# Performance work log

Hardware: AMD Instinct MI355X
Metric: run time of the kernel (lower is better)

## Reference

```python
import jax, jax.numpy as jnp
import numpy as np

FEATURE_DIM = 128
VALUE_DIM = 128


def setup_inputs() -> dict:
    key = jax.random.key(0)
    k1, k2, k3 = jax.random.split(key, 3)
    BH, S = 32, 4096
    q = jax.random.normal(k1, (BH, S, FEATURE_DIM), dtype=jnp.float32)
    k = jax.random.normal(k2, (BH, S, FEATURE_DIM), dtype=jnp.float32)
    v = jax.random.normal(k3, (BH, S, VALUE_DIM), dtype=jnp.float32)
    return {"q": q, "k": k, "v": v, "chunk_size": 128}


def reference(q, k, v, chunk_size):
    # q,k: [BH,S,F]; v: [BH,S,V]. Chunked fast-weight linear-attention scan:
    # out_t = q_t . (sum_{s<=t} k_s (x) v_s) / t
    BH, S, F = q.shape
    V = v.shape[-1]
    C = max(1, int(chunk_size))
    assert S % C == 0, "seq_len must be divisible by chunk_size for this reference"
    n_chunks = S // C
    # [n_chunks, BH, C, dim] for lax.scan over chunks
    qc = q.reshape(BH, n_chunks, C, F).transpose(1, 0, 2, 3)
    kc = k.reshape(BH, n_chunks, C, F).transpose(1, 0, 2, 3)
    vc = v.reshape(BH, n_chunks, C, V).transpose(1, 0, 2, 3)

    w0 = jnp.zeros((BH, F, V), dtype=q.dtype)

    def step(w_state, inputs):
        qi, ki, vi = inputs  # [BH,C,F], [BH,C,F], [BH,C,V]
        kv = jnp.einsum('bnf,bnv->bnfv', ki, vi)          # [BH,C,F,V]
        w_prefix = jnp.cumsum(kv, axis=1) + w_state[:, None]  # inclusive prefix sums
        out = jnp.einsum('bnf,bnfv->bnv', qi, w_prefix)    # [BH,C,V]
        return w_prefix[:, -1], out

    _, outs = jax.lax.scan(step, w0, (qc, kc, vc))
    out = outs.transpose(1, 0, 2, 3).reshape(BH, S, V)
    inv_counts = 1.0 / jnp.arange(1, S + 1, dtype=q.dtype)
    return out * inv_counts[None, :, None]
```

## Files before the change

### kernel.cpp

```cpp
#include <hip/hip_runtime.h>


typedef _Float16 f16;
typedef __attribute__((ext_vector_type(4))) _Float16 f16x4;
typedef __attribute__((ext_vector_type(8))) _Float16 f16x8;
typedef __attribute__((ext_vector_type(4))) float f32x4;
typedef __attribute__((ext_vector_type(16))) float f32x16;
typedef __attribute__((ext_vector_type(4))) float fv4;

#define MFMA32(a, b, c) __builtin_amdgcn_mfma_f32_32x32x16_f16((a), (b), (c), 0, 0, 0)

__device__ __forceinline__ int swzb(int row, int col) {
  int s = (row ^ (row >> 3)) & 7;
  return (row << 8) + ((col << 1) ^ (s << 4));
}

__device__ __forceinline__ f16x8 frag32(const f16* lds, int row, int kk, int lane) {
  int c0 = (kk << 4) + ((lane >> 5) << 3);
  return *(const f16x8*)((const char*)lds + swzb(row, c0));
}

__device__ __forceinline__ int rowf(int r, int g) {
  return (r & 3) + ((r >> 2) << 3) + (g << 2);
}

__global__ __launch_bounds__(512, 1)
void ttr_pt(const float* __restrict__ k, const float* __restrict__ v,
            f16* __restrict__ pt) {
  __shared__ f16 kT[128 * 128];
  __shared__ f16 vT[128 * 128];
  const int tid = threadIdx.x, lane = tid & 63, wave = tid >> 6;
  const int bh = blockIdx.x >> 5, c = blockIdx.x & 31;
  const float* kg = k + ((size_t)bh * 4096 + c * 128) * 128;
  const float* vg = v + ((size_t)bh * 4096 + c * 128) * 128;
  const int f0 = (tid & 31) << 2;
#pragma unroll
  for (int p = 0; p < 8; ++p) {
    int s = (p << 4) + (tid >> 5);
    fv4 xk = *(const fv4*)(kg + s * 128 + f0);
    fv4 xv = *(const fv4*)(vg + s * 128 + f0);
#pragma unroll
    for (int e = 0; e < 4; ++e) {
      *(f16*)((char*)kT + swzb(f0 + e, s)) = (f16)xk[e];
      *(f16*)((char*)vT + swzb(f0 + e, s)) = (f16)xv[e];
    }
  }
  __syncthreads();
  const int l31 = lane & 31, g = lane >> 5;
  const int mt = wave >> 1, nt0 = (wave & 1) << 1;
  f32x16 p0 = {0.f}, p1 = {0.f};
#pragma unroll
  for (int kk = 0; kk < 8; ++kk) {
    f16x8 a = frag32(vT, (mt << 5) + l31, kk, lane);
    p0 = MFMA32(a, frag32(kT, (nt0 << 5) + l31, kk, lane), p0);
    p1 = MFMA32(a, frag32(kT, ((nt0 + 1) << 5) + l31, kk, lane), p1);
  }
  f16* dst = pt + (size_t)blockIdx.x * 16384;
#pragma unroll
  for (int r = 0; r < 16; ++r) {
    int vr = (mt << 5) + rowf(r, g);
    dst[vr * 128 + (nt0 << 5) + l31] = (f16)p0[r];
    dst[vr * 128 + ((nt0 + 1) << 5) + l31] = (f16)p1[r];
  }
}

__global__ __launch_bounds__(256, 1)
void ttr_prefix(const f16* __restrict__ pt, f16* __restrict__ w) {
  __shared__ f16 xch[256 * 8];
  const int tid = threadIdx.x;
  const int bh = blockIdx.x >> 3, vs = blockIdx.x & 7;
  const int v0 = vs << 4;
  const int NT = v0 >> 5;
  const int vloc = tid >> 4, fblk = tid & 15;
  const size_t bhbase = (size_t)bh * 32 * 16384;
  const f16* src = pt + bhbase + (size_t)(v0 + vloc) * 128 + fblk * 8;
  const int kk = tid >> 5, gg = (tid >> 4) & 1, lc = tid & 15;
  f16* dstu = w + bhbase +
              (size_t)(((NT * 8 + kk) * 64) + gg * 32 + (v0 & 31) + lc) * 8;
  const int phi_w = vloc * 16 + (fblk ^ vloc);
  const int phi_r = lc * 16 + ((tid >> 4) ^ lc);
  float acc[8];
#pragma unroll
  for (int e = 0; e < 8; ++e) acc[e] = 0.f;
  for (int c = 0; c < 32; ++c) {
    f16x8 pcur = *(const f16x8*)(src + (size_t)c * 16384);
    f16x8 h;
#pragma unroll
    for (int e = 0; e < 8; ++e) h[e] = (f16)acc[e];
    *(f16x8*)(xch + phi_w * 8) = h;
    __syncthreads();
    f16x8 o = *(const f16x8*)(xch + phi_r * 8);
    *(f16x8*)(dstu + (size_t)c * 16384) = o;
    __syncthreads();
#pragma unroll
    for (int e = 0; e < 8; ++e) acc[e] += (float)pcur[e];
  }
}

__global__ __launch_bounds__(256, 3)
void ttr_out(const float* __restrict__ q, const float* __restrict__ k,
             const float* __restrict__ v, const f16* __restrict__ w,
             float* __restrict__ out) {
  __shared__ f16 s_lds[128 * 128];
  __shared__ f16 vT[32 * 128];
  __shared__ f16 w_lds[512 * 8];
  const int tid = threadIdx.x, lane = tid & 63, wave = tid >> 6;
  const int l31 = lane & 31, g = lane >> 5;
  const int widx = blockIdx.x & 31;
  const int gidx = ((blockIdx.x >> 5) << 3) + (widx & 7);
  const int vq = widx >> 3;
  const int bh = gidx >> 5, c = gidx & 31;
  const float* qg = q + ((size_t)bh * 4096 + c * 128) * 128;
  const float* kg = k + ((size_t)bh * 4096 + c * 128) * 128;
  const float* vg = v + ((size_t)bh * 4096 + c * 128) * 128 + vq * 32;

  const f16* wsrc = w + (size_t)gidx * 16384 + vq * 4096;
  f16x8 wl0 = *(const f16x8*)(wsrc + tid * 8);
  f16x8 wl1 = *(const f16x8*)(wsrc + (256 + tid) * 8);

  f16x8 qf[8];
  {
    const float* qr = qg + ((wave << 5) + l31) * 128 + (g << 3);
#pragma unroll
    for (int kk = 0; kk < 8; ++kk) {
      fv4 a = *(const fv4*)(qr + (kk << 4));
      fv4 b = *(const fv4*)(qr + (kk << 4) + 4);
      f16x8 h = {(f16)a[0], (f16)a[1], (f16)a[2], (f16)a[3],
                 (f16)b[0], (f16)b[1], (f16)b[2], (f16)b[3]};
      qf[kk] = h;
    }
  }
  {
    const int c0 = (tid & 31) << 2;
#pragma unroll
    for (int p = 0; p < 16; ++p) {
      int s = (p << 3) + (tid >> 5);
      fv4 xk = *(const fv4*)(kg + s * 128 + c0);
      f16x4 hk = {(f16)xk[0], (f16)xk[1], (f16)xk[2], (f16)xk[3]};
      *(f16x4*)((char*)s_lds + swzb(s, c0)) = hk;
    }
  }
  {
    const int c0 = (tid & 7) << 2;
#pragma unroll
    for (int p = 0; p < 4; ++p) {
      int s = (p << 5) + (tid >> 3);
      fv4 xv = *(const fv4*)(vg + s * 128 + c0);
#pragma unroll
      for (int e = 0; e < 4; ++e)
        *(f16*)((char*)vT + swzb(c0 + e, s)) = (f16)xv[e];
    }
  }
  *(f16x8*)(w_lds + tid * 8) = wl0;
  *(f16x8*)(w_lds + (256 + tid) * 8) = wl1;
  __syncthreads();

  f32x16 s0 = {0.f}, s1 = {0.f}, s2 = {0.f}, s3 = {0.f}, o0 = {0.f};
#pragma unroll
  for (int kk = 0; kk < 8; ++kk) {
    f16x8 aq = qf[kk];
    s0 = MFMA32(aq, frag32(s_lds, l31, kk, lane), s0);
    if (wave >= 1) s1 = MFMA32(aq, frag32(s_lds, 32 + l31, kk, lane), s1);
    if (wave >= 2) s2 = MFMA32(aq, frag32(s_lds, 64 + l31, kk, lane), s2);
    if (wave >= 3) s3 = MFMA32(aq, frag32(s_lds, 96 + l31, kk, lane), s3);
  }
  __syncthreads();

#define STORE_S(ACC, J)                                                       \
  {                                                                           \
    const bool dg = ((J) == wave);                                            \
    _Pragma("unroll") for (int r = 0; r < 16; ++r) {                          \
      int rl = rowf(r, g);                                                    \
      float val = ACC[r];                                                     \
      if (dg && l31 > rl) val = 0.f;                                          \
      *(f16*)((char*)s_lds + swzb((wave << 5) + rl, ((J) << 5) + l31)) =      \
          (f16)val;                                                           \
    }                                                                         \
  }
  STORE_S(s0, 0);
  if (wave >= 1) STORE_S(s1, 1);
  if (wave >= 2) STORE_S(s2, 2);
  if (wave >= 3) STORE_S(s3, 3);

#pragma unroll
  for (int kk = 0; kk < 8; ++kk)
    o0 = MFMA32(qf[kk], *(const f16x8*)(w_lds + ((kk << 6) + lane) * 8), o0);

  const int nkk = (wave + 1) << 1;
  for (int kk = 0; kk < nkk; ++kk)
    o0 = MFMA32(frag32(s_lds, (wave << 5) + l31, kk, lane),
                frag32(vT, l31, kk, lane), o0);

  float* og = out + (((size_t)bh * 4096) + c * 128 + (wave << 5)) * 128 + vq * 32;
#pragma unroll
  for (int r = 0; r < 16; ++r) {
    int rl = rowf(r, g);
    float tg = (float)(c * 128 + (wave << 5) + rl + 1);
    og[rl * 128 + l31] = o0[r] * __builtin_amdgcn_rcpf(tg);
  }
}

extern "C" void kernel_launch(void* const* d_in, const int* in_sizes, int n_in,
                              void* d_out, int out_size, void* d_ws, size_t ws_size,
                              hipStream_t stream) {
  const float* q = (const float*)d_in[0];
  const float* k = (const float*)d_in[1];
  const float* v = (const float*)d_in[2];
  float* o = (float*)d_out;
  f16* pt = (f16*)d_ws;
  f16* w = pt + (size_t)32 * 32 * 16384;
  ttr_pt<<<dim3(1024), dim3(512), 0, stream>>>(k, v, pt);
  ttr_prefix<<<dim3(256), dim3(256), 0, stream>>>(pt, w);
  ttr_out<<<dim3(4096), dim3(256), 0, stream>>>(q, k, v, w, o);
}
```

Before: 107.1 us.

## Load W fragments directly into registers, drop W LDS staging, raise occupancy

The output kernel now loads the prefix-state W fragments straight from global memory into registers, in the MFMA layout, instead of staging them through shared memory. The inter-chunk q·W product is issued before the first barrier so it overlaps with the LDS fill. Conversions to fp16 now use packed round-toward-zero cvt_pkrtz, and launch bounds ask for 4 blocks per CU instead of 3. The costs are more register pressure under the tighter bound, which could spill, and a change in rounding mode from round-to-nearest to round-toward-zero.

Measured after the change: 212.0 us. 98.0% more time.

```diff
diff --git a/kernel.cpp b/kernel.cpp
--- a/kernel.cpp
+++ b/kernel.cpp
@@ -2,13 +2,19 @@
 
 
 typedef _Float16 f16;
+typedef __attribute__((ext_vector_type(2))) _Float16 f16x2;
 typedef __attribute__((ext_vector_type(4))) _Float16 f16x4;
 typedef __attribute__((ext_vector_type(8))) _Float16 f16x8;
-typedef __attribute__((ext_vector_type(4))) float f32x4;
 typedef __attribute__((ext_vector_type(16))) float f32x16;
 typedef __attribute__((ext_vector_type(4))) float fv4;
 
 #define MFMA32(a, b, c) __builtin_amdgcn_mfma_f32_32x32x16_f16((a), (b), (c), 0, 0, 0)
+
+__device__ __forceinline__ f16x4 cvt4(fv4 x) {
+  f16x2 lo = __builtin_bit_cast(f16x2, __builtin_amdgcn_cvt_pkrtz(x[0], x[1]));
+  f16x2 hi = __builtin_bit_cast(f16x2, __builtin_amdgcn_cvt_pkrtz(x[2], x[3]));
+  return __builtin_shufflevector(lo, hi, 0, 1, 2, 3);
+}
 
 __device__ __forceinline__ int swzb(int row, int col) {
   int s = (row ^ (row >> 3)) & 7;
@@ -97,13 +103,12 @@
   }
 }
 
-__global__ __launch_bounds__(256, 3)
+__global__ __launch_bounds__(256, 4)
 void ttr_out(const float* __restrict__ q, const float* __restrict__ k,
              const float* __restrict__ v, const f16* __restrict__ w,
              float* __restrict__ out) {
   __shared__ f16 s_lds[128 * 128];
   __shared__ f16 vT[32 * 128];
-  __shared__ f16 w_lds[512 * 8];
   const int tid = threadIdx.x, lane = tid & 63, wave = tid >> 6;
   const int l31 = lane & 31, g = lane >> 5;
   const int widx = blockIdx.x & 31;
@@ -115,19 +120,19 @@
   const float* vg = v + ((size_t)bh * 4096 + c * 128) * 128 + vq * 32;
 
   const f16* wsrc = w + (size_t)gidx * 16384 + vq * 4096;
-  f16x8 wl0 = *(const f16x8*)(wsrc + tid * 8);
-  f16x8 wl1 = *(const f16x8*)(wsrc + (256 + tid) * 8);
+  f16x8 wf[8];
+#pragma unroll
+  for (int kk = 0; kk < 8; ++kk)
+    wf[kk] = *(const f16x8*)(wsrc + (size_t)((kk << 6) + lane) * 8);
 
   f16x8 qf[8];
   {
     const float* qr = qg + ((wave << 5) + l31) * 128 + (g << 3);
 #pragma unroll
     for (int kk = 0; kk < 8; ++kk) {
-      fv4 a = *(const fv4*)(qr + (kk << 4));
-      fv4 b = *(const fv4*)(qr + (kk << 4) + 4);
-      f16x8 h = {(f16)a[0], (f16)a[1], (f16)a[2], (f16)a[3],
-                 (f16)b[0], (f16)b[1], (f16)b[2], (f16)b[3]};
-      qf[kk] = h;
+      f16x4 a = cvt4(*(const fv4*)(qr + (kk << 4)));
+      f16x4 b = cvt4(*(const fv4*)(qr + (kk << 4) + 4));
+      qf[kk] = __builtin_shufflevector(a, b, 0, 1, 2, 3, 4, 5, 6, 7);
     }
   }
   {
@@ -135,9 +140,7 @@
 #pragma unroll
     for (int p = 0; p < 16; ++p) {
       int s = (p << 3) + (tid >> 5);
-      fv4 xk = *(const fv4*)(kg + s * 128 + c0);
-      f16x4 hk = {(f16)xk[0], (f16)xk[1], (f16)xk[2], (f16)xk[3]};
-      *(f16x4*)((char*)s_lds + swzb(s, c0)) = hk;
+      *(f16x4*)((char*)s_lds + swzb(s, c0)) = cvt4(*(const fv4*)(kg + s * 128 + c0));
     }
   }
   {
@@ -151,11 +154,12 @@
         *(f16*)((char*)vT + swzb(c0 + e, s)) = (f16)xv[e];
     }
   }
-  *(f16x8*)(w_lds + tid * 8) = wl0;
-  *(f16x8*)(w_lds + (256 + tid) * 8) = wl1;
+  f32x16 o0 = {0.f};
+#pragma unroll
+  for (int kk = 0; kk < 8; ++kk) o0 = MFMA32(qf[kk], wf[kk], o0);
   __syncthreads();
 
-  f32x16 s0 = {0.f}, s1 = {0.f}, s2 = {0.f}, s3 = {0.f}, o0 = {0.f};
+  f32x16 s0 = {0.f}, s1 = {0.f}, s2 = {0.f}, s3 = {0.f};
 #pragma unroll
   for (int kk = 0; kk < 8; ++kk) {
     f16x8 aq = qf[kk];
@@ -181,10 +185,6 @@
   if (wave >= 1) STORE_S(s1, 1);
   if (wave >= 2) STORE_S(s2, 2);
   if (wave >= 3) STORE_S(s3, 3);
-
-#pragma unroll
-  for (int kk = 0; kk < 8; ++kk)
-    o0 = MFMA32(qf[kk], *(const f16x8*)(w_lds + ((kk << 6) + lane) * 8), o0);
 
   const int nkk = (wave + 1) << 1;
   for (int kk = 0; kk < nkk; ++kk)
```
